# Optimization experiments

Hardware: AMD Instinct MI355X
Metric: run time of the kernel (lower is better)

## Reference

```python
import jax, jax.numpy as jnp
import numpy as np


def hsigmoid(x):
    # ReLU6(x + 3) / 6
    return jnp.clip(x + 3.0, 0.0, 6.0) / 6.0


def setup_inputs() -> dict:
    key = jax.random.key(0)
    k1, k2 = jax.random.split(key)
    B, C, H, W = 16, 256, 128, 128
    K = 7
    x = jax.random.normal(k1, (B, C, H, W), dtype=jnp.float32)
    # Kaiming-ish small init for the 2->1 7x7 conv
    conv_w = jax.random.normal(k2, (1, 2, K, K), dtype=jnp.float32) * (1.0 / np.sqrt(2 * K * K))
    conv_b = jnp.zeros((1,), dtype=jnp.float32)
    return {"x": x, "conv_w": conv_w, "conv_b": conv_b}


def reference(x, conv_w, conv_b):
    # channel-wise max and mean -> [B, 1, H, W] each
    max_x = jnp.max(x, axis=1, keepdims=True)
    avg_x = jnp.mean(x, axis=1, keepdims=True)
    out = jnp.concatenate([max_x, avg_x], axis=1)  # [B, 2, H, W]
    # 7x7 conv, stride 1, padding = k//2 (SAME for odd k)
    pad = conv_w.shape[-1] // 2
    out = jax.lax.conv_general_dilated(
        out, conv_w,
        window_strides=(1, 1),
        padding=[(pad, pad), (pad, pad)],
        dimension_numbers=("NCHW", "OIHW", "NCHW"),
    ) + conv_b[None, :, None, None]  # [B, 1, H, W]
    gate = hsigmoid(out)
    return x * gate  # broadcast over channel dim
```

## Files before the change

### kernel.cpp

```cpp
#include <hip/hip_runtime.h>
#include <math.h>

#define HW      128
#define PLANE   16384
#define CHS     256
#define BATCH   16
#define CSTRIDE 16384
#define BSTRIDE (256 * 16384)
#define CHUNK_B 8

typedef float vf4 __attribute__((ext_vector_type(4)));

__global__ __launch_bounds__(256) void reduce_kernel(
    const float* __restrict__ x, float* __restrict__ pmax, float* __restrict__ pavg,
    int b0)
{
    const int tid = threadIdx.x;
    const int sc  = tid & 31;
    const int cg  = tid >> 5;
    const int g   = blockIdx.x * 32 + sc;
    const int b   = b0 + (g >> 12);
    const int sp  = (g & 4095) << 2;

    const float* xp = x + (size_t)b * BSTRIDE + sp + (size_t)(cg << 5) * CSTRIDE;

    float4 vmax = make_float4(-INFINITY, -INFINITY, -INFINITY, -INFINITY);
    float4 vsum = make_float4(0.f, 0.f, 0.f, 0.f);

    #pragma unroll 8
    for (int c = 0; c < 32; ++c) {
        const float4 v = *(const float4*)(xp + (size_t)c * CSTRIDE);
        vmax.x = fmaxf(vmax.x, v.x); vmax.y = fmaxf(vmax.y, v.y);
        vmax.z = fmaxf(vmax.z, v.z); vmax.w = fmaxf(vmax.w, v.w);
        vsum.x += v.x; vsum.y += v.y; vsum.z += v.z; vsum.w += v.w;
    }

    __shared__ float4 smax[256];
    __shared__ float4 ssum[256];
    smax[tid] = vmax;
    ssum[tid] = vsum;
    __syncthreads();

    if (tid < 32) {
        float4 m = smax[tid];
        float4 s = ssum[tid];
        #pragma unroll
        for (int j = 1; j < 8; ++j) {
            const float4 mj = smax[tid + 32 * j];
            const float4 sj = ssum[tid + 32 * j];
            m.x = fmaxf(m.x, mj.x); m.y = fmaxf(m.y, mj.y);
            m.z = fmaxf(m.z, mj.z); m.w = fmaxf(m.w, mj.w);
            s.x += sj.x; s.y += sj.y; s.z += sj.z; s.w += sj.w;
        }
        const float inv = 1.0f / 256.0f;
        s.x *= inv; s.y *= inv; s.z *= inv; s.w *= inv;
        const int gg = blockIdx.x * 32 + tid;
        const int bb = b0 + (gg >> 12);
        const int ss = (gg & 4095) << 2;
        *(float4*)(pmax + (size_t)bb * PLANE + ss) = m;
        *(float4*)(pavg + (size_t)bb * PLANE + ss) = s;
    }
}

__global__ __launch_bounds__(256) void gate_mul_kernel(
    const float* __restrict__ x,
    const float* __restrict__ pmax, const float* __restrict__ pavg,
    const float* __restrict__ cw, const float* __restrict__ cb,
    float* __restrict__ out, int b0)
{
    __shared__ float sw[98];
    __shared__ float part[256];
    __shared__ __align__(16) float sgate[HW];

    const int tid = threadIdx.x;
    if (tid < 98) sw[tid] = cw[tid];
    const int b = b0 + (blockIdx.x >> 7);
    const int h = blockIdx.x & 127;
    __syncthreads();

    {
        const int w  = tid & 127;
        const int pl = tid >> 7;
        const float* pp = (pl ? pavg : pmax) + (size_t)b * PLANE;
        const float* wt = sw + pl * 49;
        float acc = 0.f;
        #pragma unroll
        for (int ky = 0; ky < 7; ++ky) {
            const int hh = h + ky - 3;
            if (hh >= 0 && hh < HW) {
                const float* pr = pp + hh * HW;
                #pragma unroll
                for (int kx = 0; kx < 7; ++kx) {
                    const int ww = w + kx - 3;
                    if (ww >= 0 && ww < HW)
                        acc = fmaf(wt[ky * 7 + kx], pr[ww], acc);
                }
            }
        }
        part[tid] = acc;
    }
    __syncthreads();

    if (tid < HW) {
        const float acc = part[tid] + part[tid + 128] + cb[0];
        sgate[tid] = fminf(fmaxf(acc + 3.0f, 0.0f), 6.0f) * (1.0f / 6.0f);
    }
    __syncthreads();

    const int wc   = tid & 31;
    const int csub = tid >> 5;
    const float4 g4 = *(const float4*)(sgate + wc * 4);
    const size_t rowbase = (size_t)b * BSTRIDE + (size_t)h * HW + wc * 4;

    #pragma unroll 8
    for (int c = csub; c < CHS; c += 8) {
        const size_t off = rowbase + (size_t)c * CSTRIDE;
        const float4 v = *(const float4*)(x + off);
        vf4 r;
        r.x = v.x * g4.x; r.y = v.y * g4.y; r.z = v.z * g4.z; r.w = v.w * g4.w;
        __builtin_nontemporal_store(r, (vf4*)(out + off));
    }
}

extern "C" void kernel_launch(void* const* d_in, const int* in_sizes, int n_in,
                              void* d_out, int out_size, void* d_ws, size_t ws_size,
                              hipStream_t stream)
{
    const float* x  = (const float*)d_in[0];
    const float* cw = (const float*)d_in[1];
    const float* cb = (const float*)d_in[2];
    float* out = (float*)d_out;

    float* pmax = (float*)d_ws;
    float* pavg = pmax + (size_t)BATCH * PLANE;

    for (int b0 = 0; b0 < BATCH; b0 += CHUNK_B) {
        reduce_kernel<<<CHUNK_B * 128, 256, 0, stream>>>(x, pmax, pavg, b0);
        gate_mul_kernel<<<CHUNK_B * 128, 256, 0, stream>>>(x, pmax, pavg, cw, cb, out, b0);
    }
}
```

Measured before the change: 488.8 us.

## Software-pipeline reduce and gate stages across batch chunks in merged launches

Splits the batch into chunks of four and launches combined kernels in which some blocks apply the gate to chunk s-1 while other blocks reduce chunk s. This replaces the previous serial reduce/gate pairs over chunks of eight. The goal is to keep the GPU busy across stage boundaries and to shrink the working set of each chunk so re-reads of x are more likely to hit in cache. The cost is more launches and heterogeneous blocks sharing one kernel, whose register and shared-memory usage is set by the larger of the two bodies.

```diff
diff --git a/kernel.cpp b/kernel.cpp
--- a/kernel.cpp
+++ b/kernel.cpp
@@ -7,18 +7,22 @@
 #define BATCH   16
 #define CSTRIDE 16384
 #define BSTRIDE (256 * 16384)
-#define CHUNK_B 8
+#define CB      4
+#define NCHUNK  (BATCH / CB)
 
 typedef float vf4 __attribute__((ext_vector_type(4)));
 
-__global__ __launch_bounds__(256) void reduce_kernel(
+__device__ __forceinline__ void reduce_body(
     const float* __restrict__ x, float* __restrict__ pmax, float* __restrict__ pavg,
-    int b0)
+    int b0, int rb)
 {
+    __shared__ float4 smax[256];
+    __shared__ float4 ssum[256];
+
     const int tid = threadIdx.x;
     const int sc  = tid & 31;
     const int cg  = tid >> 5;
-    const int g   = blockIdx.x * 32 + sc;
+    const int g   = rb * 32 + sc;
     const int b   = b0 + (g >> 12);
     const int sp  = (g & 4095) << 2;
 
@@ -35,8 +39,6 @@
         vsum.x += v.x; vsum.y += v.y; vsum.z += v.z; vsum.w += v.w;
     }
 
-    __shared__ float4 smax[256];
-    __shared__ float4 ssum[256];
     smax[tid] = vmax;
     ssum[tid] = vsum;
     __syncthreads();
@@ -54,7 +56,7 @@
         }
         const float inv = 1.0f / 256.0f;
         s.x *= inv; s.y *= inv; s.z *= inv; s.w *= inv;
-        const int gg = blockIdx.x * 32 + tid;
+        const int gg = rb * 32 + tid;
         const int bb = b0 + (gg >> 12);
         const int ss = (gg & 4095) << 2;
         *(float4*)(pmax + (size_t)bb * PLANE + ss) = m;
@@ -62,11 +64,11 @@
     }
 }
 
-__global__ __launch_bounds__(256) void gate_mul_kernel(
+__device__ __forceinline__ void gate_body(
     const float* __restrict__ x,
     const float* __restrict__ pmax, const float* __restrict__ pavg,
     const float* __restrict__ cw, const float* __restrict__ cb,
-    float* __restrict__ out, int b0)
+    float* __restrict__ out, int b0, int gb)
 {
     __shared__ float sw[98];
     __shared__ float part[256];
@@ -74,8 +76,8 @@
 
     const int tid = threadIdx.x;
     if (tid < 98) sw[tid] = cw[tid];
-    const int b = b0 + (blockIdx.x >> 7);
-    const int h = blockIdx.x & 127;
+    const int b = b0 + (gb >> 7);
+    const int h = gb & 127;
     __syncthreads();
 
     {
@@ -122,6 +124,33 @@
     }
 }
 
+__global__ __launch_bounds__(256) void reduce_kernel(
+    const float* __restrict__ x, float* __restrict__ pmax, float* __restrict__ pavg,
+    int b0)
+{
+    reduce_body(x, pmax, pavg, b0, blockIdx.x);
+}
+
+__global__ __launch_bounds__(256) void gate_kernel(
+    const float* __restrict__ x,
+    const float* __restrict__ pmax, const float* __restrict__ pavg,
+    const float* __restrict__ cw, const float* __restrict__ cb,
+    float* __restrict__ out, int b0)
+{
+    gate_body(x, pmax, pavg, cw, cb, out, b0, blockIdx.x);
+}
+
+__global__ __launch_bounds__(256) void mid_kernel(
+    const float* __restrict__ x, float* __restrict__ pmax, float* __restrict__ pavg,
+    const float* __restrict__ cw, const float* __restrict__ cb,
+    float* __restrict__ out, int gate_b0, int red_b0)
+{
+    if (blockIdx.x < CB * 128)
+        gate_body(x, pmax, pavg, cw, cb, out, gate_b0, blockIdx.x);
+    else
+        reduce_body(x, pmax, pavg, red_b0, blockIdx.x - CB * 128);
+}
+
 extern "C" void kernel_launch(void* const* d_in, const int* in_sizes, int n_in,
                               void* d_out, int out_size, void* d_ws, size_t ws_size,
                               hipStream_t stream)
@@ -134,8 +163,10 @@
     float* pmax = (float*)d_ws;
     float* pavg = pmax + (size_t)BATCH * PLANE;
 
-    for (int b0 = 0; b0 < BATCH; b0 += CHUNK_B) {
-        reduce_kernel<<<CHUNK_B * 128, 256, 0, stream>>>(x, pmax, pavg, b0);
-        gate_mul_kernel<<<CHUNK_B * 128, 256, 0, stream>>>(x, pmax, pavg, cw, cb, out, b0);
-    }
+    reduce_kernel<<<CB * 128, 256, 0, stream>>>(x, pmax, pavg, 0);
+    for (int s = 1; s < NCHUNK; ++s)
+        mid_kernel<<<2 * CB * 128, 256, 0, stream>>>(x, pmax, pavg, cw, cb, out,
+                                                     (s - 1) * CB, s * CB);
+    gate_kernel<<<CB * 128, 256, 0, stream>>>(x, pmax, pavg, cw, cb, out,
+                                              (NCHUNK - 1) * CB);
 }
```

New measurement: 488.2 us. No clear change (-0.1%).

## Drop batch chunking and give each block more work in reduce and gate kernels

Applied to the files above, without the earlier changes.

Replaces the two-chunk loop with one launch per kernel covering all 16 batches. In the reduction, each thread now accumulates 64 channels instead of 32 and each block covers 64 spatial quads. In the gate kernel, each block handles two rows, with each thread doing both conv planes, so the partial-sum smem pass and one barrier go away. This cuts launches and barrier overhead, but reduce now streams the full 256MB input before gate re-reads it, which may lose last-level cache reuse that chunking gave.

```diff
diff --git a/kernel.cpp b/kernel.cpp
--- a/kernel.cpp
+++ b/kernel.cpp
@@ -7,114 +7,112 @@
 #define BATCH   16
 #define CSTRIDE 16384
 #define BSTRIDE (256 * 16384)
-#define CHUNK_B 8
+
 
 typedef float vf4 __attribute__((ext_vector_type(4)));
 
-__global__ __launch_bounds__(256) void reduce_kernel(
-    const float* __restrict__ x, float* __restrict__ pmax, float* __restrict__ pavg,
-    int b0)
+__global__ __launch_bounds__(256) void reduce_all(
+    const float* __restrict__ x, float* __restrict__ pmax, float* __restrict__ pavg)
 {
+    __shared__ float4 smax[256];
+    __shared__ float4 ssum[256];
+
     const int tid = threadIdx.x;
-    const int sc  = tid & 31;
-    const int cg  = tid >> 5;
-    const int g   = blockIdx.x * 32 + sc;
-    const int b   = b0 + (g >> 12);
+    const int sc  = tid & 63;
+    const int cg  = tid >> 6;
+    const int g   = blockIdx.x * 64 + sc;
+    const int b   = g >> 12;
     const int sp  = (g & 4095) << 2;
 
-    const float* xp = x + (size_t)b * BSTRIDE + sp + (size_t)(cg << 5) * CSTRIDE;
+    const float* xp = x + (size_t)b * BSTRIDE + sp + (size_t)(cg << 6) * CSTRIDE;
 
     float4 vmax = make_float4(-INFINITY, -INFINITY, -INFINITY, -INFINITY);
     float4 vsum = make_float4(0.f, 0.f, 0.f, 0.f);
 
     #pragma unroll 8
-    for (int c = 0; c < 32; ++c) {
+    for (int c = 0; c < 64; ++c) {
         const float4 v = *(const float4*)(xp + (size_t)c * CSTRIDE);
         vmax.x = fmaxf(vmax.x, v.x); vmax.y = fmaxf(vmax.y, v.y);
         vmax.z = fmaxf(vmax.z, v.z); vmax.w = fmaxf(vmax.w, v.w);
         vsum.x += v.x; vsum.y += v.y; vsum.z += v.z; vsum.w += v.w;
     }
 
-    __shared__ float4 smax[256];
-    __shared__ float4 ssum[256];
     smax[tid] = vmax;
     ssum[tid] = vsum;
     __syncthreads();
 
-    if (tid < 32) {
+    if (tid < 64) {
         float4 m = smax[tid];
         float4 s = ssum[tid];
         #pragma unroll
-        for (int j = 1; j < 8; ++j) {
-            const float4 mj = smax[tid + 32 * j];
-            const float4 sj = ssum[tid + 32 * j];
+        for (int j = 1; j < 4; ++j) {
+            const float4 mj = smax[tid + 64 * j];
+            const float4 sj = ssum[tid + 64 * j];
             m.x = fmaxf(m.x, mj.x); m.y = fmaxf(m.y, mj.y);
             m.z = fmaxf(m.z, mj.z); m.w = fmaxf(m.w, mj.w);
             s.x += sj.x; s.y += sj.y; s.z += sj.z; s.w += sj.w;
         }
         const float inv = 1.0f / 256.0f;
         s.x *= inv; s.y *= inv; s.z *= inv; s.w *= inv;
-        const int gg = blockIdx.x * 32 + tid;
-        const int bb = b0 + (gg >> 12);
+        const int gg = blockIdx.x * 64 + tid;
+        const int bb = gg >> 12;
         const int ss = (gg & 4095) << 2;
         *(float4*)(pmax + (size_t)bb * PLANE + ss) = m;
         *(float4*)(pavg + (size_t)bb * PLANE + ss) = s;
     }
 }
 
-__global__ __launch_bounds__(256) void gate_mul_kernel(
+__global__ __launch_bounds__(256) void gate_all(
     const float* __restrict__ x,
     const float* __restrict__ pmax, const float* __restrict__ pavg,
     const float* __restrict__ cw, const float* __restrict__ cb,
-    float* __restrict__ out, int b0)
+    float* __restrict__ out)
 {
     __shared__ float sw[98];
-    __shared__ float part[256];
-    __shared__ __align__(16) float sgate[HW];
+    __shared__ __align__(16) float sgate[2][HW];
 
     const int tid = threadIdx.x;
     if (tid < 98) sw[tid] = cw[tid];
-    const int b = b0 + (blockIdx.x >> 7);
-    const int h = blockIdx.x & 127;
+    const int b  = blockIdx.x >> 6;
+    const int hp = blockIdx.x & 63;
+    const int h0 = hp << 1;
     __syncthreads();
 
     {
         const int w  = tid & 127;
-        const int pl = tid >> 7;
-        const float* pp = (pl ? pavg : pmax) + (size_t)b * PLANE;
-        const float* wt = sw + pl * 49;
-        float acc = 0.f;
+        const int rs = tid >> 7;
+        const int h  = h0 + rs;
+        float acc = cb[0];
         #pragma unroll
-        for (int ky = 0; ky < 7; ++ky) {
-            const int hh = h + ky - 3;
-            if (hh >= 0 && hh < HW) {
-                const float* pr = pp + hh * HW;
-                #pragma unroll
-                for (int kx = 0; kx < 7; ++kx) {
-                    const int ww = w + kx - 3;
-                    if (ww >= 0 && ww < HW)
-                        acc = fmaf(wt[ky * 7 + kx], pr[ww], acc);
+        for (int pl = 0; pl < 2; ++pl) {
+            const float* pp = (pl ? pavg : pmax) + (size_t)b * PLANE;
+            const float* wt = sw + pl * 49;
+            #pragma unroll
+            for (int ky = 0; ky < 7; ++ky) {
+                const int hh = h + ky - 3;
+                if (hh >= 0 && hh < HW) {
+                    const float* pr = pp + hh * HW;
+                    #pragma unroll
+                    for (int kx = 0; kx < 7; ++kx) {
+                        const int ww = w + kx - 3;
+                        if (ww >= 0 && ww < HW)
+                            acc = fmaf(wt[ky * 7 + kx], pr[ww], acc);
+                    }
                 }
             }
         }
-        part[tid] = acc;
+        sgate[rs][w] = fminf(fmaxf(acc + 3.0f, 0.0f), 6.0f) * (1.0f / 6.0f);
     }
     __syncthreads();
 
-    if (tid < HW) {
-        const float acc = part[tid] + part[tid + 128] + cb[0];
-        sgate[tid] = fminf(fmaxf(acc + 3.0f, 0.0f), 6.0f) * (1.0f / 6.0f);
-    }
-    __syncthreads();
-
-    const int wc   = tid & 31;
-    const int csub = tid >> 5;
-    const float4 g4 = *(const float4*)(sgate + wc * 4);
-    const size_t rowbase = (size_t)b * BSTRIDE + (size_t)h * HW + wc * 4;
+    const int l    = tid & 63;
+    const int csub = tid >> 6;
+    const float4 g4 = *(const float4*)(&sgate[l >> 5][(l & 31) * 4]);
+    const size_t spanbase = (size_t)b * BSTRIDE + (size_t)h0 * HW + l * 4;
 
     #pragma unroll 8
-    for (int c = csub; c < CHS; c += 8) {
-        const size_t off = rowbase + (size_t)c * CSTRIDE;
+    for (int c = csub; c < CHS; c += 4) {
+        const size_t off = spanbase + (size_t)c * CSTRIDE;
         const float4 v = *(const float4*)(x + off);
         vf4 r;
         r.x = v.x * g4.x; r.y = v.y * g4.y; r.z = v.z * g4.z; r.w = v.w * g4.w;
@@ -134,8 +132,6 @@
     float* pmax = (float*)d_ws;
     float* pavg = pmax + (size_t)BATCH * PLANE;
 
-    for (int b0 = 0; b0 < BATCH; b0 += CHUNK_B) {
-        reduce_kernel<<<CHUNK_B * 128, 256, 0, stream>>>(x, pmax, pavg, b0);
-        gate_mul_kernel<<<CHUNK_B * 128, 256, 0, stream>>>(x, pmax, pavg, cw, cb, out, b0);
-    }
+    reduce_all<<<1024, 256, 0, stream>>>(x, pmax, pavg);
+    gate_all<<<1024, 256, 0, stream>>>(x, pmax, pavg, cw, cb, out);
 }
```

After: 484.3 us (median of 2 runs). Within noise of the previous version (-0.9%).
